# Optimization experiments

Hardware: AMD Instinct MI355X
Metric: run time of the kernel (lower is better)

The kernel has to match this reference:

```python
import jax, jax.numpy as jnp
import numpy as np


def setup_inputs() -> dict:
    key = jax.random.key(0)
    k1, k2 = jax.random.split(key)
    x = jax.random.normal(k1, (2, 256, 512, 512), dtype=jnp.float32)
    # torch.rand -> uniform [0, 1)
    kernel = jax.random.uniform(k2, (1, 256, 11, 11), dtype=jnp.float32)
    bias = jnp.zeros((1,), dtype=jnp.float32)
    return {"x": x, "kernel": kernel, "bias": bias}


def reference(x, kernel, bias):
    # Faithful to the original: output[:, 0, i, j] = sum over BATCH, channels,
    # and kernel window of (patch * kernel), i.e. the reduction includes the
    # batch dim, and the same scalar map is broadcast to every batch element.
    # sum_b(patch_b) == patch(sum_b x), so this collapses to one VALID conv
    # over the batch-summed input.
    B = x.shape[0]
    xs = jnp.sum(x, axis=0, keepdims=True)  # [1, C, H, W]
    out = jax.lax.conv_general_dilated(
        xs, kernel,
        window_strides=(1, 1),
        padding='VALID',
        dimension_numbers=('NCHW', 'OIHW', 'NCHW'),
    )  # [1, 1, O, O]
    out = jnp.broadcast_to(out, (B,) + out.shape[1:])  # [B, 1, O, O]
    return out + bias  # bias (1,) broadcasts over all dims
```

## Files before the change

kernel.cpp:

```cpp
#include <hip/hip_runtime.h>

#define H   512
#define W   512
#define C   256
#define KH  11
#define KW  11
#define OH  502
#define OW  502
#define OUT_MAP (OH * OW)

#define TX 4
#define TY 4
#define TILE_X 64
#define TILE_Y 64
#define IN_X  (TILE_X + KW - 1)
#define IN_Y  (TILE_Y + KH - 1)
#define IN_XP 76
#define CPB   32
#define VEC_PER_ROW 19

__global__ __launch_bounds__(256, 2)
void conv_kernel(const float* __restrict__ x, const float* __restrict__ w,
                 float* __restrict__ out)
{
    __shared__ float s_in[IN_Y * IN_XP];

    const int tid = threadIdx.x;
    const int tx  = tid & 15;
    const int ty  = tid >> 4;
    const int x0  = blockIdx.x * TILE_X;
    const int y0  = blockIdx.y * TILE_Y;
    const int c0  = blockIdx.z * CPB;

    float acc[TY][TX];
#pragma unroll
    for (int dy = 0; dy < TY; ++dy)
#pragma unroll
        for (int i = 0; i < TX; ++i) acc[dy][i] = 0.f;

    const int ry0 = ty * TY;
    const int cx0 = tx * TX;

    for (int cc = 0; cc < CPB; ++cc) {
        const int c = c0 + cc;
        const float* __restrict__ xb0 = x + (size_t)c * (H * W);
        const float* __restrict__ xb1 = xb0 + (size_t)C * H * W;

        for (int i = tid; i < IN_Y * VEC_PER_ROW; i += 256) {
            const int row = i / VEC_PER_ROW;
            const int vec = i - row * VEC_PER_ROW;
            const int gy  = y0 + row;
            const int gx  = x0 + vec * 4;
            float4 v = make_float4(0.f, 0.f, 0.f, 0.f);
            if (gy < H) {
                if (gx + 3 < W) {
                    const float4 a = *(const float4*)(xb0 + (size_t)gy * W + gx);
                    const float4 b = *(const float4*)(xb1 + (size_t)gy * W + gx);
                    v = make_float4(a.x + b.x, a.y + b.y, a.z + b.z, a.w + b.w);
                } else {
                    float t[4] = {0.f, 0.f, 0.f, 0.f};
#pragma unroll
                    for (int j = 0; j < 4; ++j)
                        if (gx + j < W)
                            t[j] = xb0[(size_t)gy * W + gx + j] + xb1[(size_t)gy * W + gx + j];
                    v = make_float4(t[0], t[1], t[2], t[3]);
                }
            }
            *(float4*)&s_in[row * IN_XP + vec * 4] = v;
        }
        __syncthreads();

        const float* __restrict__ wc = w + (size_t)c * (KH * KW);
#pragma unroll
        for (int r = 0; r < TY + KH - 1; ++r) {
            const float* rp = &s_in[(ry0 + r) * IN_XP + cx0];
            const float4 a0 = *(const float4*)(rp + 0);
            const float4 a1 = *(const float4*)(rp + 4);
            const float4 a2 = *(const float4*)(rp + 8);
            const float4 a3 = *(const float4*)(rp + 12);
            const float win[16] = {a0.x, a0.y, a0.z, a0.w,
                                   a1.x, a1.y, a1.z, a1.w,
                                   a2.x, a2.y, a2.z, a2.w,
                                   a3.x, a3.y, a3.z, a3.w};
#pragma unroll
            for (int dy = 0; dy < TY; ++dy) {
                const int kh = r - dy;
                if (kh >= 0 && kh < KH) {
#pragma unroll
                    for (int kw = 0; kw < KW; ++kw) {
                        const float wv = wc[kh * KW + kw];
#pragma unroll
                        for (int i = 0; i < TX; ++i)
                            acc[dy][i] += win[kw + i] * wv;
                    }
                }
            }
        }
        __syncthreads();
    }

#pragma unroll
    for (int dy = 0; dy < TY; ++dy) {
        const int oy = y0 + ry0 + dy;
        if (oy < OH) {
#pragma unroll
            for (int i = 0; i < TX; ++i) {
                const int ox = x0 + cx0 + i;
                if (ox < OW)
                    atomicAdd(&out[(size_t)oy * OW + ox], acc[dy][i]);
            }
        }
    }
}

__global__ void init_kernel(float* __restrict__ out, const float* __restrict__ bias)
{
    const int i = blockIdx.x * 256 + threadIdx.x;
    if (i < OUT_MAP) out[i] = bias[0];
}

__global__ void bcast_kernel(float* __restrict__ out)
{
    const int i = blockIdx.x * 256 + threadIdx.x;
    if (i < OUT_MAP) out[OUT_MAP + i] = out[i];
}

extern "C" void kernel_launch(void* const* d_in, const int* in_sizes, int n_in,
                              void* d_out, int out_size, void* d_ws, size_t ws_size,
                              hipStream_t stream)
{
    const float* x    = (const float*)d_in[0];
    const float* w    = (const float*)d_in[1];
    const float* bias = (const float*)d_in[2];
    float* out = (float*)d_out;

    const int nb = (OUT_MAP + 255) / 256;
    init_kernel<<<nb, 256, 0, stream>>>(out, bias);
    conv_kernel<<<dim3(8, 8, 8), 256, 0, stream>>>(x, w, out);
    bcast_kernel<<<nb, 256, 0, stream>>>(out);
}
```

Before: 946.5 us.

## Split channels across more blocks and precompute staging offsets with clamped loads

Reduces channels per block from 32 to 8 and quadruples the grid in z, so 2048 blocks are launched instead of 512 to better fill the GPU. Raises the launch-bounds occupancy target to 7 blocks per SM. Precomputes the per-thread global and shared offsets for tile staging once, with clamped coordinates that replace the per-element bounds branches. The cost is four times as many atomic adds into the output, tighter register limits, and out-of-range halo cells filled with clamped data instead of zeros; those cells only feed outputs that are never written.

```diff
diff --git a/kernel.cpp b/kernel.cpp
--- a/kernel.cpp
+++ b/kernel.cpp
@@ -8,6 +8,7 @@
 #define OH  502
 #define OW  502
 #define OUT_MAP (OH * OW)
+#define HWSZ (H * W)
 
 #define TX 4
 #define TY 4
@@ -16,10 +17,12 @@
 #define IN_X  (TILE_X + KW - 1)
 #define IN_Y  (TILE_Y + KH - 1)
 #define IN_XP 76
-#define CPB   32
+#define CPB   8
 #define VEC_PER_ROW 19
+#define NSTAGE_TOT (IN_Y * VEC_PER_ROW)
+#define NSTAGE_IT  6
 
-__global__ __launch_bounds__(256, 2)
+__global__ __launch_bounds__(256, 7)
 void conv_kernel(const float* __restrict__ x, const float* __restrict__ w,
                  float* __restrict__ out)
 {
@@ -32,6 +35,23 @@
     const int y0  = blockIdx.y * TILE_Y;
     const int c0  = blockIdx.z * CPB;
 
+    int s_goff[NSTAGE_IT];
+    int s_loff[NSTAGE_IT];
+    bool s_act[NSTAGE_IT];
+#pragma unroll
+    for (int j = 0; j < NSTAGE_IT; ++j) {
+        int i = tid + j * 256;
+        const bool act = (i < NSTAGE_TOT);
+        if (!act) i = 0;
+        const int row = i / VEC_PER_ROW;
+        const int vec = i - row * VEC_PER_ROW;
+        const int gy  = min(y0 + row, H - 1);
+        const int gx  = min(x0 + vec * 4, W - 4);
+        s_goff[j] = gy * W + gx;
+        s_loff[j] = row * IN_XP + vec * 4;
+        s_act[j]  = act;
+    }
+
     float acc[TY][TX];
 #pragma unroll
     for (int dy = 0; dy < TY; ++dy)
@@ -43,30 +63,17 @@
 
     for (int cc = 0; cc < CPB; ++cc) {
         const int c = c0 + cc;
-        const float* __restrict__ xb0 = x + (size_t)c * (H * W);
-        const float* __restrict__ xb1 = xb0 + (size_t)C * H * W;
+        const float* __restrict__ p0 = x + (size_t)c * HWSZ;
+        const float* __restrict__ p1 = p0 + (size_t)C * HWSZ;
 
-        for (int i = tid; i < IN_Y * VEC_PER_ROW; i += 256) {
-            const int row = i / VEC_PER_ROW;
-            const int vec = i - row * VEC_PER_ROW;
-            const int gy  = y0 + row;
-            const int gx  = x0 + vec * 4;
-            float4 v = make_float4(0.f, 0.f, 0.f, 0.f);
-            if (gy < H) {
-                if (gx + 3 < W) {
-                    const float4 a = *(const float4*)(xb0 + (size_t)gy * W + gx);
-                    const float4 b = *(const float4*)(xb1 + (size_t)gy * W + gx);
-                    v = make_float4(a.x + b.x, a.y + b.y, a.z + b.z, a.w + b.w);
-                } else {
-                    float t[4] = {0.f, 0.f, 0.f, 0.f};
 #pragma unroll
-                    for (int j = 0; j < 4; ++j)
-                        if (gx + j < W)
-                            t[j] = xb0[(size_t)gy * W + gx + j] + xb1[(size_t)gy * W + gx + j];
-                    v = make_float4(t[0], t[1], t[2], t[3]);
-                }
+        for (int j = 0; j < NSTAGE_IT; ++j) {
+            if (s_act[j]) {
+                const float4 a = *(const float4*)(p0 + s_goff[j]);
+                const float4 b = *(const float4*)(p1 + s_goff[j]);
+                *(float4*)&s_in[s_loff[j]] =
+                    make_float4(a.x + b.x, a.y + b.y, a.z + b.z, a.w + b.w);
             }
-            *(float4*)&s_in[row * IN_XP + vec * 4] = v;
         }
         __syncthreads();
 
@@ -136,6 +143,6 @@
 
     const int nb = (OUT_MAP + 255) / 256;
     init_kernel<<<nb, 256, 0, stream>>>(out, bias);
-    conv_kernel<<<dim3(8, 8, 8), 256, 0, stream>>>(x, w, out);
+    conv_kernel<<<dim3(8, 8, 32), 256, 0, stream>>>(x, w, out);
     bcast_kernel<<<nb, 256, 0, stream>>>(out);
 }
```

After: 829.1 us. 1.14x faster.
